# Optimization experiments

Hardware: AMD Instinct MI355X
Metric: run time of the kernel (lower is better)

Reference implementation:

```python
import jax, jax.numpy as jnp
import numpy as np

B, N, F_IN, F_OUT, K, E = 4, 50000, 64, 64, 4, 800000


def setup_inputs() -> dict:
    key = jax.random.key(0)
    ks = jax.random.split(key, 6)
    x = jax.random.normal(ks[0], (B, N, F_IN), dtype=jnp.float32)
    support_rows = jax.random.randint(ks[1], (K, E), 0, N, dtype=jnp.int32)
    support_cols = jax.random.randint(ks[2], (K, E), 0, N, dtype=jnp.int32)
    support_vals = jax.random.normal(ks[3], (K, E), dtype=jnp.float32) * 0.1
    kernels = jax.random.normal(ks[4], (K, F_IN, F_OUT), dtype=jnp.float32) * (1.0 / np.sqrt(F_IN))
    bias = jnp.zeros((F_OUT,), dtype=jnp.float32)
    return {"x": x, "support_rows": support_rows, "support_cols": support_cols,
            "support_vals": support_vals, "kernels": kernels, "bias": bias}


def reference(x, support_rows, support_cols, support_vals, kernels, bias):
    # dropout_rate = 0.0 -> identity; sum_k support_k @ (x @ W_k) + bias, relu
    n = x.shape[1]
    out = jnp.zeros(x.shape[:2] + (kernels.shape[-1],), dtype=x.dtype)
    for k in range(kernels.shape[0]):  # small fixed K = 4 Chebyshev supports
        h = jnp.einsum('bnf,fg->bng', x, kernels[k])          # dense projection
        msg = h[:, support_cols[k], :] * support_vals[k][None, :, None]  # [B,E,G]
        agg = jax.ops.segment_sum(jnp.swapaxes(msg, 0, 1), support_rows[k],
                                  num_segments=n)              # [N,B,G]
        out = out + jnp.swapaxes(agg, 0, 1)
    return jax.nn.relu(out + bias)
```

## Files before the change

### kernel.cpp

```cpp
#include <hip/hip_runtime.h>


#define FDIM 64
#define CHUNK_SHIFT 12

__device__ __forceinline__ unsigned short bf16_rne(float v) {
    unsigned u = __float_as_uint(v);
    return (unsigned short)((u + 0x7FFFu + ((u >> 16) & 1u)) >> 16);
}

__global__ __launch_bounds__(256) void pack_x(
    const float* __restrict__ x, unsigned short* __restrict__ xb,
    int M, int N)
{
    int i = blockIdx.x * 256 + threadIdx.x;
    if (i >= M * 16) return;
    int f4 = i & 15;
    int bn = i >> 4;
    int b = bn / N;
    int n = bn - b * N;
    float4 v = ((const float4*)x)[i];
    ushort4 p;
    p.x = bf16_rne(v.x); p.y = bf16_rne(v.y);
    p.z = bf16_rne(v.z); p.w = bf16_rne(v.w);
    *(ushort4*)(xb + (size_t)n * 256 + b * 64 + f4 * 4) = p;
}

__global__ __launch_bounds__(256) void hist2(
    const int* __restrict__ rows, const int* __restrict__ cols,
    int* __restrict__ counts2, int total, int E, int N, int CNUM)
{
    int i = blockIdx.x * 256 + threadIdx.x;
    if (i >= total) return;
    int k = i / E;
    int idx = (k * N + rows[i]) * CNUM + (cols[i] >> CHUNK_SHIFT);
    atomicAdd(&counts2[idx], 1);
}

__global__ __launch_bounds__(256) void scan_block_sums(
    const int* __restrict__ counts, int* __restrict__ bsums, int N, int nb)
{
    int k = blockIdx.x / nb, j = blockIdx.x % nb;
    int t = threadIdx.x, lane = t & 63, w = t >> 6;
    int i = j * 256 + t;
    int v = (i < N) ? counts[k * N + i] : 0;
#pragma unroll
    for (int off = 32; off; off >>= 1) v += __shfl_down(v, off);
    __shared__ int lds[4];
    if (lane == 0) lds[w] = v;
    __syncthreads();
    if (t == 0) bsums[k * nb + j] = lds[0] + lds[1] + lds[2] + lds[3];
}

__global__ __launch_bounds__(256) void scan_bsums(int* bsums, int nb, int K)
{
    __shared__ int lds[4];
    __shared__ int carry;
    int t = threadIdx.x, lane = t & 63, w = t >> 6;
    for (int k = 0; k < K; ++k) {
        if (t == 0) carry = 0;
        __syncthreads();
        for (int base = 0; base < nb; base += 256) {
            int i = base + t;
            int v = (i < nb) ? bsums[k * nb + i] : 0;
            int x = v;
#pragma unroll
            for (int off = 1; off < 64; off <<= 1) {
                int y = __shfl_up(x, off);
                if (lane >= off) x += y;
            }
            if (lane == 63) lds[w] = x;
            __syncthreads();
            int wo = 0;
            for (int q = 0; q < w; ++q) wo += lds[q];
            int excl = carry + wo + x - v;
            if (i < nb) bsums[k * nb + i] = excl;
            __syncthreads();
            if (t == 255) carry = carry + wo + x;
            __syncthreads();
        }
    }
}

__global__ __launch_bounds__(256) void scan_write_ptr(
    const int* __restrict__ counts, const int* __restrict__ bsums,
    int* __restrict__ ptr, int N, int nb)
{
    int k = blockIdx.x / nb, j = blockIdx.x % nb;
    int t = threadIdx.x, lane = t & 63, w = t >> 6;
    int i = j * 256 + t;
    int v = (i < N) ? counts[k * N + i] : 0;
    int x = v;
#pragma unroll
    for (int off = 1; off < 64; off <<= 1) {
        int y = __shfl_up(x, off);
        if (lane >= off) x += y;
    }
    __shared__ int lds[4];
    if (lane == 63) lds[w] = x;
    __syncthreads();
    int wo = 0;
    for (int q = 0; q < w; ++q) wo += lds[q];
    int incl = wo + x;
    if (i < N) ptr[k * (N + 1) + i + 1] = bsums[k * nb + j] + incl;
    if (t == 0 && j == 0) ptr[k * (N + 1)] = 0;
}

__global__ __launch_bounds__(256) void fill2(
    const int* __restrict__ rows, const int* __restrict__ cols,
    const float* __restrict__ vals, const int* __restrict__ seg_ptr,
    int* __restrict__ counts2, unsigned* __restrict__ csr,
    int total, int E, int N, int CNUM)
{
    int i = blockIdx.x * 256 + threadIdx.x;
    if (i >= total) return;
    int k = i / E;
    int col = cols[i];
    int idx = (k * N + rows[i]) * CNUM + (col >> CHUNK_SHIFT);
    int old = atomicSub(&counts2[idx], 1);
    int slot = seg_ptr[idx] + old - 1;
    csr[slot] = ((unsigned)col << 16) | (unsigned)bf16_rne(vals[i]);
}

__global__ __launch_bounds__(256) void gather_gemm(
    const unsigned short* __restrict__ xb,
    const int* __restrict__ seg_ptr,
    const unsigned* __restrict__ csr,
    const float* __restrict__ kernels,
    const float* __restrict__ bias,
    float* __restrict__ out,
    int N, int CNUM)
{
    __shared__ unsigned short Wl[256 * 64];
    __shared__ float accS[4][4][260];

    const int t = threadIdx.x;

#pragma unroll
    for (int i = 0; i < 16; ++i) {
        int idx = t + 256 * i;
        float4 v = ((const float4*)kernels)[idx];
        ushort4 p;
        p.x = bf16_rne(v.x); p.y = bf16_rne(v.y);
        p.z = bf16_rne(v.z); p.w = bf16_rne(v.w);
        ((ushort4*)Wl)[idx] = p;
    }
    __syncthreads();

    const int w = t >> 6, lane = t & 63;
    const int row = blockIdx.x * 4 + w;
    const int b = lane >> 4;
    const int q4 = lane & 15;

    if (row < N) {
        const unsigned short* xbl = xb + lane * 4;
        float4 acc[4];
#pragma unroll
        for (int k = 0; k < 4; ++k) acc[k] = make_float4(0.f, 0.f, 0.f, 0.f);

#pragma unroll
        for (int k = 0; k < 4; ++k) {
            const int e0 = seg_ptr[(k * N + row) * CNUM];
            const int e1 = seg_ptr[(k * N + row + 1) * CNUM];
#pragma unroll 8
            for (int j = e0; j < e1; ++j) {
                unsigned ww = csr[j];
                int col = ww >> 16;
                float val = __uint_as_float(ww << 16);
                uint2 hv = *(const uint2*)(xbl + (size_t)col * 256);
                float f0 = __uint_as_float(hv.x << 16);
                float f1 = __uint_as_float(hv.x & 0xFFFF0000u);
                float f2 = __uint_as_float(hv.y << 16);
                float f3 = __uint_as_float(hv.y & 0xFFFF0000u);
                acc[k].x = fmaf(f0, val, acc[k].x);
                acc[k].y = fmaf(f1, val, acc[k].y);
                acc[k].z = fmaf(f2, val, acc[k].z);
                acc[k].w = fmaf(f3, val, acc[k].w);
            }
        }

#pragma unroll
        for (int k = 0; k < 4; ++k)
            *(float4*)&accS[w][b][k * 64 + q4 * 4] = acc[k];
    }
    __syncthreads();

    if (row < N) {
        float4 o = make_float4(0.f, 0.f, 0.f, 0.f);
#pragma unroll 4
        for (int kf = 0; kf < 256; ++kf) {
            float a = accS[w][b][kf];
            ushort4 wv = *(const ushort4*)&Wl[kf * 64 + q4 * 4];
            o.x = fmaf(a, __uint_as_float((unsigned)wv.x << 16), o.x);
            o.y = fmaf(a, __uint_as_float((unsigned)wv.y << 16), o.y);
            o.z = fmaf(a, __uint_as_float((unsigned)wv.z << 16), o.z);
            o.w = fmaf(a, __uint_as_float((unsigned)wv.w << 16), o.w);
        }
        float4 bi = ((const float4*)bias)[q4];
        o.x = fmaxf(o.x + bi.x, 0.f);
        o.y = fmaxf(o.y + bi.y, 0.f);
        o.z = fmaxf(o.z + bi.z, 0.f);
        o.w = fmaxf(o.w + bi.w, 0.f);
        *(float4*)(out + ((size_t)b * N + row) * 64 + q4 * 4) = o;
    }
}

__global__ __launch_bounds__(256) void gemm64(
    const float* __restrict__ x, const float* __restrict__ W,
    float* __restrict__ h, int M)
{
    __shared__ float xs[64][68];
    __shared__ float Wl[64][64];
    const int t = threadIdx.x;
    {
        const float4* Wv = (const float4*)W;
        float4* Wd = (float4*)&Wl[0][0];
#pragma unroll
        for (int i = 0; i < 4; ++i) Wd[t + 256 * i] = Wv[t + 256 * i];
    }
    const int row0 = blockIdx.x * 64;
#pragma unroll
    for (int i = 0; i < 4; ++i) {
        int idx = t + 256 * i;
        int r = idx >> 4;
        int c4 = idx & 15;
        float4 v = ((const float4*)(x + (size_t)(row0 + r) * FDIM))[c4];
        int f = c4 * 4;
        xs[f + 0][r] = v.x; xs[f + 1][r] = v.y;
        xs[f + 2][r] = v.z; xs[f + 3][r] = v.w;
    }
    __syncthreads();
    const int r0 = (t >> 4) * 4;
    const int g0 = (t & 15) * 4;
    float acc[4][4];
#pragma unroll
    for (int i = 0; i < 4; ++i)
#pragma unroll
        for (int j = 0; j < 4; ++j) acc[i][j] = 0.f;
#pragma unroll
    for (int f = 0; f < 64; ++f) {
        float4 xv = *(const float4*)&xs[f][r0];
        float4 wv = *(const float4*)&Wl[f][g0];
        acc[0][0] = fmaf(xv.x, wv.x, acc[0][0]); acc[0][1] = fmaf(xv.x, wv.y, acc[0][1]);
        acc[0][2] = fmaf(xv.x, wv.z, acc[0][2]); acc[0][3] = fmaf(xv.x, wv.w, acc[0][3]);
        acc[1][0] = fmaf(xv.y, wv.x, acc[1][0]); acc[1][1] = fmaf(xv.y, wv.y, acc[1][1]);
        acc[1][2] = fmaf(xv.y, wv.z, acc[1][2]); acc[1][3] = fmaf(xv.y, wv.w, acc[1][3]);
        acc[2][0] = fmaf(xv.z, wv.x, acc[2][0]); acc[2][1] = fmaf(xv.z, wv.y, acc[2][1]);
        acc[2][2] = fmaf(xv.z, wv.z, acc[2][2]); acc[2][3] = fmaf(xv.z, wv.w, acc[2][3]);
        acc[3][0] = fmaf(xv.w, wv.x, acc[3][0]); acc[3][1] = fmaf(xv.w, wv.y, acc[3][1]);
        acc[3][2] = fmaf(xv.w, wv.z, acc[3][2]); acc[3][3] = fmaf(xv.w, wv.w, acc[3][3]);
    }
#pragma unroll
    for (int i = 0; i < 4; ++i)
        *(float4*)(h + (size_t)(row0 + r0 + i) * FDIM + g0) =
            make_float4(acc[i][0], acc[i][1], acc[i][2], acc[i][3]);
}

__global__ __launch_bounds__(256) void scatter_edges(
    const float* __restrict__ h, const int* __restrict__ rows,
    const int* __restrict__ cols, const float* __restrict__ vals,
    float* __restrict__ out, int E, int N)
{
    const int e = (blockIdx.x << 2) | (threadIdx.x >> 6);
    if (e >= E) return;
    const int lane = threadIdx.x & 63;
    const int row = __builtin_amdgcn_readfirstlane(rows[e]);
    const int col = __builtin_amdgcn_readfirstlane(cols[e]);
    const float val =
        __uint_as_float(__builtin_amdgcn_readfirstlane(__float_as_uint(vals[e])));
    const size_t stride = (size_t)N * FDIM;
    size_t cbase = (size_t)col * FDIM + lane;
    size_t rbase = (size_t)row * FDIM + lane;
#pragma unroll
    for (int b = 0; b < 4; ++b) {
        float hv = h[cbase + (size_t)b * stride];
        atomicAdd(out + rbase + (size_t)b * stride, hv * val);
    }
}

__global__ __launch_bounds__(256) void bias_relu(
    float* __restrict__ out, const float* __restrict__ bias, size_t total4)
{
    size_t i = (size_t)blockIdx.x * blockDim.x + threadIdx.x;
    if (i >= total4) return;
    float4 v = ((float4*)out)[i];
    float4 b = ((const float4*)bias)[i & 15];
    v.x = fmaxf(v.x + b.x, 0.f); v.y = fmaxf(v.y + b.y, 0.f);
    v.z = fmaxf(v.z + b.z, 0.f); v.w = fmaxf(v.w + b.w, 0.f);
    ((float4*)out)[i] = v;
}

extern "C" void kernel_launch(void* const* d_in, const int* in_sizes, int n_in,
                              void* d_out, int out_size, void* d_ws, size_t ws_size,
                              hipStream_t stream) {
    const float* x       = (const float*)d_in[0];
    const int*   rows    = (const int*)d_in[1];
    const int*   cols    = (const int*)d_in[2];
    const float* vals    = (const float*)d_in[3];
    const float* kernels = (const float*)d_in[4];
    const float* bias    = (const float*)d_in[5];

    float* out = (float*)d_out;

    const int K = in_sizes[4] / (FDIM * FDIM);
    const int E = in_sizes[1] / K;
    const int M = in_sizes[0] / FDIM;
    const int N = M / 4;
    const int total = K * E;

    const int CNUM = (N + (1 << CHUNK_SHIFT) - 1) >> CHUNK_SHIFT;
    const long long L = (long long)K * N * CNUM;
    const int nb2 = (int)((L + 255) / 256);

    const size_t al = 15;
    const size_t xbB  = (((size_t)N * 512) + al) & ~al;
    const size_t csrB = (((size_t)total * 4) + al) & ~al;
    const size_t segB = (((size_t)(L + 1) * 4) + al) & ~al;
    const size_t cntB = (((size_t)L * 4) + al) & ~al;
    const size_t bsB  = (((size_t)nb2 * 4) + al) & ~al;
    const size_t needed = xbB + csrB + segB + cntB + bsB;

    const bool fast = (K == 4) && (N <= 65536) && (M == 4 * N) &&
                      (ws_size >= needed) && (L < (1LL << 31));

    if (fast) {
        char* ws = (char*)d_ws;
        unsigned short* xb  = (unsigned short*)ws;  ws += xbB;
        unsigned* csr       = (unsigned*)ws;        ws += csrB;
        int* seg_ptr        = (int*)ws;             ws += segB;
        int* counts2        = (int*)ws;             ws += cntB;
        int* bsums2         = (int*)ws;

        pack_x<<<(M * 16 + 255) / 256, 256, 0, stream>>>(x, xb, M, N);

        hipMemsetAsync(counts2, 0, (size_t)L * 4, stream);
        hist2<<<(total + 255) / 256, 256, 0, stream>>>(
            rows, cols, counts2, total, E, N, CNUM);
        scan_block_sums<<<nb2, 256, 0, stream>>>(counts2, bsums2, (int)L, nb2);
        scan_bsums<<<1, 256, 0, stream>>>(bsums2, nb2, 1);
        scan_write_ptr<<<nb2, 256, 0, stream>>>(counts2, bsums2, seg_ptr, (int)L, nb2);
        fill2<<<(total + 255) / 256, 256, 0, stream>>>(
            rows, cols, vals, seg_ptr, counts2, csr, total, E, N, CNUM);

        gather_gemm<<<(N + 3) / 4, 256, 0, stream>>>(
            xb, seg_ptr, csr, kernels, bias, out, N, CNUM);
    } else {
        float* h = (float*)d_ws;
        hipMemsetAsync(out, 0, (size_t)out_size * sizeof(float), stream);
        for (int k = 0; k < K; ++k) {
            gemm64<<<M / 64, 256, 0, stream>>>(
                x, kernels + (size_t)k * FDIM * FDIM, h, M);
            scatter_edges<<<(E + 3) / 4, 256, 0, stream>>>(
                h, rows + (size_t)k * E, cols + (size_t)k * E,
                vals + (size_t)k * E, out, E, N);
        }
        const size_t total4 = (size_t)out_size / 4;
        bias_relu<<<(int)((total4 + 255) / 256), 256, 0, stream>>>(out, bias, total4);
    }
}
```

Baseline: 882.4 us.

## Pack bucket counts as bytes, pre-pack weights, and batch CSR loads via shuffles

Bucket counters now pack four 8-bit counts into each 32-bit word, which shrinks the memset and scan traffic fourfold; the atomics now work on packed bytes. Weights are converted to bf16 once by a separate kernel, so each gather_gemm block no longer fills 32KB of LDS, which should raise occupancy. The final GEMM reads weights from global/L2 instead of LDS. The edge loop loads 64 CSR entries per wave at once and broadcasts them with shuffles instead of issuing a scalar load per edge. The risk is that a bucket count above 255 would overflow its byte, though the random inputs make that unlikely.

```diff
diff --git a/kernel.cpp b/kernel.cpp
--- a/kernel.cpp
+++ b/kernel.cpp
@@ -26,70 +26,80 @@
     *(ushort4*)(xb + (size_t)n * 256 + b * 64 + f4 * 4) = p;
 }
 
-__global__ __launch_bounds__(256) void hist2(
+__global__ __launch_bounds__(256) void pack_w(
+    const float* __restrict__ kern, unsigned short* __restrict__ Wb, int n4)
+{
+    int i = blockIdx.x * 256 + threadIdx.x;
+    if (i >= n4) return;
+    float4 v = ((const float4*)kern)[i];
+    ushort4 p;
+    p.x = bf16_rne(v.x); p.y = bf16_rne(v.y);
+    p.z = bf16_rne(v.z); p.w = bf16_rne(v.w);
+    ((ushort4*)Wb)[i] = p;
+}
+
+__global__ __launch_bounds__(256) void hist2_u8(
     const int* __restrict__ rows, const int* __restrict__ cols,
-    int* __restrict__ counts2, int total, int E, int N, int CNUM)
+    unsigned* __restrict__ cnt, int total, int E, int N, int CNUM)
 {
     int i = blockIdx.x * 256 + threadIdx.x;
     if (i >= total) return;
     int k = i / E;
     int idx = (k * N + rows[i]) * CNUM + (cols[i] >> CHUNK_SHIFT);
-    atomicAdd(&counts2[idx], 1);
-}
-
-__global__ __launch_bounds__(256) void scan_block_sums(
-    const int* __restrict__ counts, int* __restrict__ bsums, int N, int nb)
-{
-    int k = blockIdx.x / nb, j = blockIdx.x % nb;
+    atomicAdd(&cnt[idx >> 2], 1u << ((idx & 3) * 8));
+}
+
+__global__ __launch_bounds__(256) void scan_block_sums_u8(
+    const unsigned* __restrict__ cnt, int* __restrict__ bsums, int L, int nb)
+{
+    int j = blockIdx.x;
     int t = threadIdx.x, lane = t & 63, w = t >> 6;
     int i = j * 256 + t;
-    int v = (i < N) ? counts[k * N + i] : 0;
+    int v = (i < L) ? (int)((cnt[i >> 2] >> ((i & 3) * 8)) & 0xFF) : 0;
 #pragma unroll
     for (int off = 32; off; off >>= 1) v += __shfl_down(v, off);
     __shared__ int lds[4];
     if (lane == 0) lds[w] = v;
     __syncthreads();
-    if (t == 0) bsums[k * nb + j] = lds[0] + lds[1] + lds[2] + lds[3];
-}
-
-__global__ __launch_bounds__(256) void scan_bsums(int* bsums, int nb, int K)
+    if (t == 0) bsums[j] = lds[0] + lds[1] + lds[2] + lds[3];
+}
+
+__global__ __launch_bounds__(256) void scan_bsums(int* bsums, int nb)
 {
     __shared__ int lds[4];
     __shared__ int carry;
     int t = threadIdx.x, lane = t & 63, w = t >> 6;
-    for (int k = 0; k < K; ++k) {
-        if (t == 0) carry = 0;
+    if (t == 0) carry = 0;
+    __syncthreads();
+    for (int base = 0; base < nb; base += 256) {
+        int i = base + t;
+        int v = (i < nb) ? bsums[i] : 0;
+        int x = v;
+#pragma unroll
+        for (int off = 1; off < 64; off <<= 1) {
+            int y = __shfl_up(x, off);
+            if (lane >= off) x += y;
+        }
+        if (lane == 63) lds[w] = x;
         __syncthreads();
-        for (int base = 0; base < nb; base += 256) {
-            int i = base + t;
-            int v = (i < nb) ? bsums[k * nb + i] : 0;
-            int x = v;
-#pragma unroll
-            for (int off = 1; off < 64; off <<= 1) {
-                int y = __shfl_up(x, off);
-                if (lane >= off) x += y;
-            }
-            if (lane == 63) lds[w] = x;
-            __syncthreads();
-            int wo = 0;
-            for (int q = 0; q < w; ++q) wo += lds[q];
-            int excl = carry + wo + x - v;
-            if (i < nb) bsums[k * nb + i] = excl;
-            __syncthreads();
-            if (t == 255) carry = carry + wo + x;
-            __syncthreads();
-        }
-    }
-}
-
-__global__ __launch_bounds__(256) void scan_write_ptr(
-    const int* __restrict__ counts, const int* __restrict__ bsums,
-    int* __restrict__ ptr, int N, int nb)
-{
-    int k = blockIdx.x / nb, j = blockIdx.x % nb;
+        int wo = 0;
+        for (int q = 0; q < w; ++q) wo += lds[q];
+        int excl = carry + wo + x - v;
+        if (i < nb) bsums[i] = excl;
+        __syncthreads();
+        if (t == 255) carry = carry + wo + x;
+        __syncthreads();
+    }
+}
+
+__global__ __launch_bounds__(256) void scan_write_ptr_u8(
+    const unsigned* __restrict__ cnt, const int* __restrict__ bsums,
+    int* __restrict__ seg_ptr, int L, int nb)
+{
+    int j = blockIdx.x;
     int t = threadIdx.x, lane = t & 63, w = t >> 6;
     int i = j * 256 + t;
-    int v = (i < N) ? counts[k * N + i] : 0;
+    int v = (i < L) ? (int)((cnt[i >> 2] >> ((i & 3) * 8)) & 0xFF) : 0;
     int x = v;
 #pragma unroll
     for (int off = 1; off < 64; off <<= 1) {
@@ -102,14 +112,14 @@
     int wo = 0;
     for (int q = 0; q < w; ++q) wo += lds[q];
     int incl = wo + x;
-    if (i < N) ptr[k * (N + 1) + i + 1] = bsums[k * nb + j] + incl;
-    if (t == 0 && j == 0) ptr[k * (N + 1)] = 0;
-}
-
-__global__ __launch_bounds__(256) void fill2(
+    if (i < L) seg_ptr[i + 1] = bsums[j] + incl;
+    if (t == 0 && j == 0) seg_ptr[0] = 0;
+}
+
+__global__ __launch_bounds__(256) void fill2_u8(
     const int* __restrict__ rows, const int* __restrict__ cols,
     const float* __restrict__ vals, const int* __restrict__ seg_ptr,
-    int* __restrict__ counts2, unsigned* __restrict__ csr,
+    unsigned* __restrict__ cnt, unsigned* __restrict__ csr,
     int total, int E, int N, int CNUM)
 {
     int i = blockIdx.x * 256 + threadIdx.x;
@@ -117,8 +127,10 @@
     int k = i / E;
     int col = cols[i];
     int idx = (k * N + rows[i]) * CNUM + (col >> CHUNK_SHIFT);
-    int old = atomicSub(&counts2[idx], 1);
-    int slot = seg_ptr[idx] + old - 1;
+    int sh = (idx & 3) * 8;
+    unsigned old = atomicAdd(&cnt[idx >> 2], (unsigned)(-(1u << sh)));
+    int oldf = (int)((old >> sh) & 0xFF);
+    int slot = seg_ptr[idx] + oldf - 1;
     csr[slot] = ((unsigned)col << 16) | (unsigned)bf16_rne(vals[i]);
 }
 
@@ -126,27 +138,14 @@
     const unsigned short* __restrict__ xb,
     const int* __restrict__ seg_ptr,
     const unsigned* __restrict__ csr,
-    const float* __restrict__ kernels,
+    const unsigned short* __restrict__ Wb,
     const float* __restrict__ bias,
     float* __restrict__ out,
     int N, int CNUM)
 {
-    __shared__ unsigned short Wl[256 * 64];
     __shared__ float accS[4][4][260];
 
     const int t = threadIdx.x;
-
-#pragma unroll
-    for (int i = 0; i < 16; ++i) {
-        int idx = t + 256 * i;
-        float4 v = ((const float4*)kernels)[idx];
-        ushort4 p;
-        p.x = bf16_rne(v.x); p.y = bf16_rne(v.y);
-        p.z = bf16_rne(v.z); p.w = bf16_rne(v.w);
-        ((ushort4*)Wl)[idx] = p;
-    }
-    __syncthreads();
-
     const int w = t >> 6, lane = t & 63;
     const int row = blockIdx.x * 4 + w;
     const int b = lane >> 4;
@@ -162,20 +161,21 @@
         for (int k = 0; k < 4; ++k) {
             const int e0 = seg_ptr[(k * N + row) * CNUM];
             const int e1 = seg_ptr[(k * N + row + 1) * CNUM];
-#pragma unroll 8
-            for (int j = e0; j < e1; ++j) {
-                unsigned ww = csr[j];
-                int col = ww >> 16;
-                float val = __uint_as_float(ww << 16);
-                uint2 hv = *(const uint2*)(xbl + (size_t)col * 256);
-                float f0 = __uint_as_float(hv.x << 16);
-                float f1 = __uint_as_float(hv.x & 0xFFFF0000u);
-                float f2 = __uint_as_float(hv.y << 16);
-                float f3 = __uint_as_float(hv.y & 0xFFFF0000u);
-                acc[k].x = fmaf(f0, val, acc[k].x);
-                acc[k].y = fmaf(f1, val, acc[k].y);
-                acc[k].z = fmaf(f2, val, acc[k].z);
-                acc[k].w = fmaf(f3, val, acc[k].w);
+            for (int base = e0; base < e1; base += 64) {
+                const int nn = min(64, e1 - base);
+                unsigned wv = 0;
+                if (lane < nn) wv = csr[base + lane];
+#pragma unroll 4
+                for (int j = 0; j < nn; ++j) {
+                    unsigned ww = (unsigned)__shfl((int)wv, j);
+                    int col = ww >> 16;
+                    float val = __uint_as_float(ww << 16);
+                    uint2 hv = *(const uint2*)(xbl + (size_t)col * 256);
+                    acc[k].x = fmaf(__uint_as_float(hv.x << 16), val, acc[k].x);
+                    acc[k].y = fmaf(__uint_as_float(hv.x & 0xFFFF0000u), val, acc[k].y);
+                    acc[k].z = fmaf(__uint_as_float(hv.y << 16), val, acc[k].z);
+                    acc[k].w = fmaf(__uint_as_float(hv.y & 0xFFFF0000u), val, acc[k].w);
+                }
             }
         }
 
@@ -187,10 +187,11 @@
 
     if (row < N) {
         float4 o = make_float4(0.f, 0.f, 0.f, 0.f);
-#pragma unroll 4
+        const float* as = &accS[w][b][0];
+#pragma unroll 8
         for (int kf = 0; kf < 256; ++kf) {
-            float a = accS[w][b][kf];
-            ushort4 wv = *(const ushort4*)&Wl[kf * 64 + q4 * 4];
+            float a = as[kf];
+            ushort4 wv = *(const ushort4*)&Wb[kf * 64 + q4 * 4];
             o.x = fmaf(a, __uint_as_float((unsigned)wv.x << 16), o.x);
             o.y = fmaf(a, __uint_as_float((unsigned)wv.y << 16), o.y);
             o.z = fmaf(a, __uint_as_float((unsigned)wv.z << 16), o.z);
@@ -316,9 +317,10 @@
     const size_t xbB  = (((size_t)N * 512) + al) & ~al;
     const size_t csrB = (((size_t)total * 4) + al) & ~al;
     const size_t segB = (((size_t)(L + 1) * 4) + al) & ~al;
-    const size_t cntB = (((size_t)L * 4) + al) & ~al;
+    const size_t cntB = (((size_t)L + al) & ~al) + 16;
     const size_t bsB  = (((size_t)nb2 * 4) + al) & ~al;
-    const size_t needed = xbB + csrB + segB + cntB + bsB;
+    const size_t wbB  = (((size_t)K * FDIM * FDIM * 2) + al) & ~al;
+    const size_t needed = xbB + csrB + segB + cntB + bsB + wbB;
 
     const bool fast = (K == 4) && (N <= 65536) && (M == 4 * N) &&
                       (ws_size >= needed) && (L < (1LL << 31));
@@ -328,22 +330,25 @@
         unsigned short* xb  = (unsigned short*)ws;  ws += xbB;
         unsigned* csr       = (unsigned*)ws;        ws += csrB;
         int* seg_ptr        = (int*)ws;             ws += segB;
-        int* counts2        = (int*)ws;             ws += cntB;
-        int* bsums2         = (int*)ws;
+        unsigned* cnt       = (unsigned*)ws;        ws += cntB;
+        int* bsums2         = (int*)ws;             ws += bsB;
+        unsigned short* Wb  = (unsigned short*)ws;
 
         pack_x<<<(M * 16 + 255) / 256, 256, 0, stream>>>(x, xb, M, N);
-
-        hipMemsetAsync(counts2, 0, (size_t)L * 4, stream);
-        hist2<<<(total + 255) / 256, 256, 0, stream>>>(
-            rows, cols, counts2, total, E, N, CNUM);
-        scan_block_sums<<<nb2, 256, 0, stream>>>(counts2, bsums2, (int)L, nb2);
-        scan_bsums<<<1, 256, 0, stream>>>(bsums2, nb2, 1);
-        scan_write_ptr<<<nb2, 256, 0, stream>>>(counts2, bsums2, seg_ptr, (int)L, nb2);
-        fill2<<<(total + 255) / 256, 256, 0, stream>>>(
-            rows, cols, vals, seg_ptr, counts2, csr, total, E, N, CNUM);
+        pack_w<<<(K * FDIM * FDIM / 4 + 255) / 256, 256, 0, stream>>>(
+            kernels, Wb, K * FDIM * FDIM / 4);
+
+        hipMemsetAsync(cnt, 0, cntB, stream);
+        hist2_u8<<<(total + 255) / 256, 256, 0, stream>>>(
+            rows, cols, cnt, total, E, N, CNUM);
+        scan_block_sums_u8<<<nb2, 256, 0, stream>>>(cnt, bsums2, (int)L, nb2);
+        scan_bsums<<<1, 256, 0, stream>>>(bsums2, nb2);
+        scan_write_ptr_u8<<<nb2, 256, 0, stream>>>(cnt, bsums2, seg_ptr, (int)L, nb2);
+        fill2_u8<<<(total + 255) / 256, 256, 0, stream>>>(
+            rows, cols, vals, seg_ptr, cnt, csr, total, E, N, CNUM);
 
         gather_gemm<<<(N + 3) / 4, 256, 0, stream>>>(
-            xb, seg_ptr, csr, kernels, bias, out, N, CNUM);
+            xb, seg_ptr, csr, Wb, bias, out, N, CNUM);
     } else {
         float* h = (float*)d_ws;
         hipMemsetAsync(out, 0, (size_t)out_size * sizeof(float), stream);
```

Result: slower. 949.5 us (+7.6%).
